# Optimization experiments

Measured on AMD Instinct MI355X. Metric: run time of the kernel, lower is better.

## Reference

```python
import jax, jax.numpy as jnp
import numpy as np

LEAKY_ALPHA = 0.2  # tf.nn.leaky_relu default

def setup_inputs() -> dict:
    key = jax.random.key(0)
    k1, k2, k3 = jax.random.split(key, 3)
    B, N, F, U = 4, 4096, 128, 64
    x = jax.random.normal(k1, (B, N, F), dtype=jnp.float32)
    W = jax.random.normal(k2, (F, U), dtype=jnp.float32) * (1.0 / np.sqrt(F))
    a = jax.random.normal(k3, (2 * U, 1), dtype=jnp.float32) * (1.0 / np.sqrt(2 * U))
    return {"x": x, "W": W, "a": a}

def reference(x, W, a):
    # h: (B, N, U)
    h = jnp.einsum('bnf,fu->bnu', x, W)
    U = h.shape[-1]
    a1 = a[:U, 0]   # attends to source node i
    a2 = a[U:, 0]   # attends to target node j
    # a^T [h_i || h_j] = a1^T h_i + a2^T h_j  (same math, no O(N^2*2U) concat)
    f1 = jnp.einsum('bnu,u->bn', h, a1)  # (B, N)
    f2 = jnp.einsum('bnu,u->bn', h, a2)  # (B, N)
    e = f1[:, :, None] + f2[:, None, :]  # (B, N, N)
    e = jnp.where(e >= 0, e, LEAKY_ALPHA * e)
    attn = jax.nn.softmax(e, axis=-1)    # softmax over j
    return jnp.einsum('bij,bju->biu', attn, h)
```

## Files before the change

### kernel.cpp

```cpp
#include <hip/hip_runtime.h>
#include <hip/hip_bf16.h>

#define NBATCH 4
#define NN 4096
#define NF 128
#define NU 64
#define CH 16
#define NCH (NN / CH)
#define LEAKY 0.2f

__global__ __launch_bounds__(256) void k1_h(
    const float* __restrict__ x, const float* __restrict__ W,
    const float* __restrict__ a,
    float* __restrict__ h, float* __restrict__ f1, float* __restrict__ f2) {
  int tid = threadIdx.x;
  int u = tid & 63;
  int wv = tid >> 6;
  int row0 = __builtin_amdgcn_readfirstlane(blockIdx.x * 16 + wv * 4);
  const float* xb = x + (size_t)row0 * NF;
  float acc[4] = {0.f, 0.f, 0.f, 0.f};
#pragma unroll
  for (int ft = 0; ft < NF; ft += 32) {
    float w[32];
#pragma unroll
    for (int i = 0; i < 32; ++i) w[i] = W[(ft + i) * NU + u];
#pragma unroll
    for (int r = 0; r < 4; ++r) {
      const float* xr = xb + r * NF + ft;
#pragma unroll
      for (int i = 0; i < 32; ++i) acc[r] += xr[i] * w[i];
    }
  }
  float a1 = a[u], a2 = a[NU + u];
#pragma unroll
  for (int r = 0; r < 4; ++r) {
    int grow = row0 + r;
    h[(size_t)grow * NU + u] = acc[r];
    float p1 = acc[r] * a1, p2 = acc[r] * a2;
#pragma unroll
    for (int off = 32; off >= 1; off >>= 1) {
      p1 += __shfl_xor(p1, off, 64);
      p2 += __shfl_xor(p2, off, 64);
    }
    if (u == 0) { f1[grow] = p1; f2[grow] = p2; }
  }
}

__global__ __launch_bounds__(256) void k2a_count(
    const float* __restrict__ f2, unsigned short* __restrict__ pc) {
  __shared__ float fsk[256];
  int b = blockIdx.x >> 7;
  int jc = (blockIdx.x >> 4) & 7;
  int kc = blockIdx.x & 15;
  int tid = threadIdx.x;
  const float* f2b = f2 + b * NN;
  fsk[tid] = f2b[kc * 256 + tid];
  __syncthreads();
  int j0 = jc * 512 + tid;
  int j1 = j0 + 256;
  float my0 = f2b[j0], my1 = f2b[j1];
  int k0g = kc * 256;
  int cnt0 = 0, cnt1 = 0;
#pragma unroll 8
  for (int k = 0; k < 256; k += 4) {
    float4 v = *(const float4*)&fsk[k];
    int kg = k0g + k;
    cnt0 += (v.x < my0) || (v.x == my0 && kg + 0 < j0);
    cnt0 += (v.y < my0) || (v.y == my0 && kg + 1 < j0);
    cnt0 += (v.z < my0) || (v.z == my0 && kg + 2 < j0);
    cnt0 += (v.w < my0) || (v.w == my0 && kg + 3 < j0);
    cnt1 += (v.x < my1) || (v.x == my1 && kg + 0 < j1);
    cnt1 += (v.y < my1) || (v.y == my1 && kg + 1 < j1);
    cnt1 += (v.z < my1) || (v.z == my1 && kg + 2 < j1);
    cnt1 += (v.w < my1) || (v.w == my1 && kg + 3 < j1);
  }
  size_t base = ((size_t)(b * 16 + kc)) * NN;
  pc[base + j0] = (unsigned short)cnt0;
  pc[base + j1] = (unsigned short)cnt1;
}

__global__ __launch_bounds__(256) void k2b_scatter(
    const float* __restrict__ f2, const unsigned short* __restrict__ pc,
    float4* __restrict__ sdat, float* __restrict__ f2s) {
  int b = blockIdx.x >> 4;
  int jc = blockIdx.x & 15;
  int j = jc * 256 + threadIdx.x;
  float my = f2[b * NN + j];
  int rank = 0;
#pragma unroll
  for (int kc = 0; kc < 16; ++kc)
    rank += pc[((size_t)(b * 16 + kc)) * NN + j];
  int o = b * NN + rank;
  float4 v;
  v.x = my; v.y = expf(my); v.z = expf(LEAKY * my); v.w = __int_as_float(j);
  sdat[o] = v;
  f2s[o] = my;
}

__global__ __launch_bounds__(256) void k3_csum(
    const float* __restrict__ h, const float4* __restrict__ sdat,
    float* __restrict__ Pvhi, float* __restrict__ Pvlo,
    float* __restrict__ Pshi, float* __restrict__ Pslo) {
  int u = threadIdx.x & 63;
  int wv = threadIdx.x >> 6;
  int cg = blockIdx.x * 4 + wv;
  int b = cg >> 8;
  int c = cg & (NCH - 1);
  int k0 = b * NN + c * CH;
  const float* hb = h + (size_t)b * NN * NU;
  float ah = 0.f, al = 0.f, sh = 0.f, sl = 0.f;
#pragma unroll
  for (int k = 0; k < CH; ++k) {
    float4 e = sdat[k0 + k];
    int j = __float_as_int(e.w);
    float hv = hb[(size_t)j * NU + u];
    ah += e.y * hv; al += e.z * hv; sh += e.y; sl += e.z;
  }
  size_t o = (size_t)(b * (NCH + 1) + c) * NU + u;
  Pvhi[o] = ah; Pvlo[o] = al;
  if (u == 0) { Pshi[b * (NCH + 1) + c] = sh; Pslo[b * (NCH + 1) + c] = sl; }
}

__global__ __launch_bounds__(256) void k3b_scan(
    float* __restrict__ Pvhi, float* __restrict__ Pvlo,
    float* __restrict__ Pshi, float* __restrict__ Pslo) {
  int wid = blockIdx.x * 4 + (threadIdx.x >> 6);
  int l = threadIdx.x & 63;
  if (wid < 512) {
    int b = wid >> 7;
    int half = (wid >> 6) & 1;
    int u = wid & 63;
    float* T = half ? Pvlo : Pvhi;
    size_t i0 = (size_t)(b * (NCH + 1) + 4 * l) * NU + u;
    float v0 = T[i0], v1 = T[i0 + NU], v2 = T[i0 + 2*NU], v3 = T[i0 + 3*NU];
    float lsum = v0 + v1 + v2 + v3, s = lsum;
#pragma unroll
    for (int off = 1; off < 64; off <<= 1) {
      float t = __shfl_up(s, off, 64);
      if (l >= off) s += t;
    }
    float e = s - lsum;
    T[i0] = e;
    T[i0 + NU] = e + v0;
    T[i0 + 2*NU] = e + v0 + v1;
    T[i0 + 3*NU] = e + v0 + v1 + v2;
    if (l == 63) T[(size_t)(b * (NCH + 1) + NCH) * NU + u] = s;
  } else if (wid < 520) {
    int s2 = wid - 512;
    int b = s2 >> 1;
    float* T = (s2 & 1) ? Pslo : Pshi;
    int i0 = b * (NCH + 1) + 4 * l;
    float v0 = T[i0], v1 = T[i0 + 1], v2 = T[i0 + 2], v3 = T[i0 + 3];
    float lsum = v0 + v1 + v2 + v3, s = lsum;
#pragma unroll
    for (int off = 1; off < 64; off <<= 1) {
      float t = __shfl_up(s, off, 64);
      if (l >= off) s += t;
    }
    float e = s - lsum;
    T[i0] = e; T[i0 + 1] = e + v0; T[i0 + 2] = e + v0 + v1;
    T[i0 + 3] = e + v0 + v1 + v2;
    if (l == 63) T[b * (NCH + 1) + NCH] = s;
  }
}

__global__ __launch_bounds__(256) void k4_out(
    const float* __restrict__ f1, const float* __restrict__ f2s,
    const float* __restrict__ h, const float4* __restrict__ sdat,
    const float* __restrict__ Pvhi, const float* __restrict__ Pvlo,
    const float* __restrict__ Pshi, const float* __restrict__ Pslo,
    float* __restrict__ out) {
  int u = threadIdx.x & 63;
  int wv = threadIdx.x >> 6;
  int row = blockIdx.x * 4 + wv;
  int b = row >> 12;
  const float* fs = f2s + b * NN;
  float fv = f1[row];
  float theta = -fv;
  float q1 = fs[u * 64 + 63];
  int n1 = __popcll(__ballot(q1 < theta));
  int t;
  if (n1 == 64) {
    t = NN;
  } else {
    float q2 = fs[n1 * 64 + u];
    t = n1 * 64 + __popcll(__ballot(q2 < theta));
  }
  int c = t >> 4; if (c > NCH - 1) c = NCH - 1;
  int k0 = b * NN + c * CH;
  const float* hb = h + (size_t)b * NN * NU;
  float ch = 0.f, cl = 0.f, csh = 0.f, csl = 0.f;
#pragma unroll
  for (int k = 0; k < CH; ++k) {
    int kg = c * CH + k;
    float4 e = sdat[k0 + k];
    int j = __float_as_int(e.w);
    float hv = hb[(size_t)j * NU + u];
    bool hi = (kg >= t);
    float wH = hi ? e.y : 0.f;
    float wL = hi ? 0.f : e.z;
    ch += wH * hv; cl += wL * hv; csh += wH; csl += wL;
  }
  size_t base = (size_t)b * (NCH + 1);
  size_t oc0 = (base + c) * NU + u;
  size_t oc1 = (base + c + 1) * NU + u;
  size_t oT  = (base + NCH) * NU + u;
  float Ahi = (Pvhi[oT] - Pvhi[oc1]) + ch;
  float Alo = Pvlo[oc0] + cl;
  float Shi = (Pshi[base + NCH] - Pshi[base + c + 1]) + csh;
  float Slo = Pslo[base + c] + csl;
  float e1 = expf(fv), e1l = expf(LEAKY * fv);
  float den = e1 * Shi + e1l * Slo;
  out[(size_t)row * NU + u] = (e1 * Ahi + e1l * Alo) / den;
}

extern "C" void kernel_launch(void* const* d_in, const int* in_sizes, int n_in,
                              void* d_out, int out_size, void* d_ws, size_t ws_size,
                              hipStream_t stream) {
  const float* x = (const float*)d_in[0];
  const float* W = (const float*)d_in[1];
  const float* a = (const float*)d_in[2];
  float* out = (float*)d_out;
  float* ws = (float*)d_ws;

  size_t o = 0;
  float* h    = ws + o; o += (size_t)NBATCH * NN * NU;
  float* f1   = ws + o; o += (size_t)NBATCH * NN;
  float* f2   = ws + o; o += (size_t)NBATCH * NN;
  float* f2s  = ws + o; o += (size_t)NBATCH * NN;
  float4* sdat = (float4*)(ws + o); o += (size_t)NBATCH * NN * 4;
  float* Pvhi = ws + o; o += (size_t)NBATCH * (NCH + 1) * NU;
  float* Pvlo = ws + o; o += (size_t)NBATCH * (NCH + 1) * NU;
  float* Pshi = ws + o; o += (size_t)NBATCH * (NCH + 1);
  float* Pslo = ws + o; o += (size_t)NBATCH * (NCH + 1);
  unsigned short* pc = (unsigned short*)(ws + o); o += (size_t)NBATCH * 16 * NN / 2;

  k1_h<<<(NBATCH * NN) / 16, 256, 0, stream>>>(x, W, a, h, f1, f2);
  k2a_count<<<512, 256, 0, stream>>>(f2, pc);
  k2b_scatter<<<NBATCH * 16, 256, 0, stream>>>(f2, pc, sdat, f2s);
  k3_csum<<<(NBATCH * NCH) / 4, 256, 0, stream>>>(h, sdat, Pvhi, Pvlo, Pshi, Pslo);
  k3b_scan<<<130, 256, 0, stream>>>(Pvhi, Pvlo, Pshi, Pslo);
  k4_out<<<(NBATCH * NN) / 4, 256, 0, stream>>>(f1, f2s, h, sdat,
      Pvhi, Pvlo, Pshi, Pslo, out);
}
```

Before: 128.3 us.

## Remap projection kernel to row-per-lane tiling and widen scatter grid

The projection kernel is remapped so each lane owns one node row and each wave computes 16 output units. x is read as float4 per lane, W loads become wave-uniform (scalar/broadcast), h is stored as float4, and the f1/f2 dot products are reduced through shared memory instead of 64-lane shuffles. The rank-scatter kernel is relaunched with 64-thread blocks and 256 blocks so more CUs are busy. The new mapping makes per-lane x loads strided by a full row, which may hurt coalescing, and the 16-wide accumulators raise register use.

```diff
diff --git a/kernel.cpp b/kernel.cpp
--- a/kernel.cpp
+++ b/kernel.cpp
@@ -13,36 +13,48 @@
     const float* __restrict__ x, const float* __restrict__ W,
     const float* __restrict__ a,
     float* __restrict__ h, float* __restrict__ f1, float* __restrict__ f2) {
+  __shared__ float p1s[4][64], p2s[4][64];
   int tid = threadIdx.x;
-  int u = tid & 63;
-  int wv = tid >> 6;
-  int row0 = __builtin_amdgcn_readfirstlane(blockIdx.x * 16 + wv * 4);
-  const float* xb = x + (size_t)row0 * NF;
-  float acc[4] = {0.f, 0.f, 0.f, 0.f};
-#pragma unroll
-  for (int ft = 0; ft < NF; ft += 32) {
-    float w[32];
-#pragma unroll
-    for (int i = 0; i < 32; ++i) w[i] = W[(ft + i) * NU + u];
-#pragma unroll
-    for (int r = 0; r < 4; ++r) {
-      const float* xr = xb + r * NF + ft;
-#pragma unroll
-      for (int i = 0; i < 32; ++i) acc[r] += xr[i] * w[i];
+  int lane = tid & 63;
+  int wv = __builtin_amdgcn_readfirstlane(tid >> 6);
+  int u0 = wv * 16;
+  int row = blockIdx.x * 64 + lane;
+  const float* xr = x + (size_t)row * NF;
+  float acc[16];
+#pragma unroll
+  for (int i = 0; i < 16; ++i) acc[i] = 0.f;
+#pragma unroll 8
+  for (int f = 0; f < NF; f += 4) {
+    float4 xv = *(const float4*)(xr + f);
+#pragma unroll
+    for (int i = 0; i < 4; ++i) {
+      const float* wr = W + (size_t)(f + i) * NU + u0;
+      float xf = (i == 0) ? xv.x : (i == 1) ? xv.y : (i == 2) ? xv.z : xv.w;
+#pragma unroll
+      for (int uu = 0; uu < 16; ++uu)
+        acc[uu] += xf * wr[uu];
     }
   }
-  float a1 = a[u], a2 = a[NU + u];
-#pragma unroll
-  for (int r = 0; r < 4; ++r) {
-    int grow = row0 + r;
-    h[(size_t)grow * NU + u] = acc[r];
-    float p1 = acc[r] * a1, p2 = acc[r] * a2;
-#pragma unroll
-    for (int off = 32; off >= 1; off >>= 1) {
-      p1 += __shfl_xor(p1, off, 64);
-      p2 += __shfl_xor(p2, off, 64);
-    }
-    if (u == 0) { f1[grow] = p1; f2[grow] = p2; }
+  float* hr = h + (size_t)row * NU + u0;
+#pragma unroll
+  for (int q = 0; q < 4; ++q) {
+    float4 v;
+    v.x = acc[4*q+0]; v.y = acc[4*q+1]; v.z = acc[4*q+2]; v.w = acc[4*q+3];
+    *(float4*)(hr + 4*q) = v;
+  }
+  float p1 = 0.f, p2 = 0.f;
+#pragma unroll
+  for (int uu = 0; uu < 16; ++uu) {
+    p1 += acc[uu] * a[u0 + uu];
+    p2 += acc[uu] * a[NU + u0 + uu];
+  }
+  p1s[wv][lane] = p1;
+  p2s[wv][lane] = p2;
+  __syncthreads();
+  if (tid < 64) {
+    int grow = blockIdx.x * 64 + tid;
+    f1[grow] = p1s[0][tid] + p1s[1][tid] + p1s[2][tid] + p1s[3][tid];
+    f2[grow] = p2s[0][tid] + p2s[1][tid] + p2s[2][tid] + p2s[3][tid];
   }
 }
 
@@ -79,12 +91,12 @@
   pc[base + j1] = (unsigned short)cnt1;
 }
 
-__global__ __launch_bounds__(256) void k2b_scatter(
+__global__ __launch_bounds__(64) void k2b_scatter(
     const float* __restrict__ f2, const unsigned short* __restrict__ pc,
     float4* __restrict__ sdat, float* __restrict__ f2s) {
-  int b = blockIdx.x >> 4;
-  int jc = blockIdx.x & 15;
-  int j = jc * 256 + threadIdx.x;
+  int g = blockIdx.x * 64 + threadIdx.x;
+  int b = g >> 12;
+  int j = g & (NN - 1);
   float my = f2[b * NN + j];
   int rank = 0;
 #pragma unroll
@@ -235,9 +247,9 @@
   float* Pslo = ws + o; o += (size_t)NBATCH * (NCH + 1);
   unsigned short* pc = (unsigned short*)(ws + o); o += (size_t)NBATCH * 16 * NN / 2;
 
-  k1_h<<<(NBATCH * NN) / 16, 256, 0, stream>>>(x, W, a, h, f1, f2);
+  k1_h<<<(NBATCH * NN) / 64, 256, 0, stream>>>(x, W, a, h, f1, f2);
   k2a_count<<<512, 256, 0, stream>>>(f2, pc);
-  k2b_scatter<<<NBATCH * 16, 256, 0, stream>>>(f2, pc, sdat, f2s);
+  k2b_scatter<<<(NBATCH * NN) / 64, 64, 0, stream>>>(f2, pc, sdat, f2s);
   k3_csum<<<(NBATCH * NCH) / 4, 256, 0, stream>>>(h, sdat, Pvhi, Pvlo, Pshi, Pslo);
   k3b_scan<<<130, 256, 0, stream>>>(Pvhi, Pvlo, Pshi, Pslo);
   k4_out<<<(NBATCH * NN) / 4, 256, 0, stream>>>(f1, f2s, h, sdat,
```

After: 113.3 us. -11.7%, faster.
